# Kernel optimization log

Measured on AMD Instinct MI355X. Metric: run time of the kernel, lower is better.

The kernel has to match this reference:

```python
import math
import jax, jax.numpy as jnp
import numpy as np

C = 64
GRID = 2

def _conv1x1(x, W, b):
    # 1x1 conv == channel-mixing matmul: [B,C,H,W] x [O,C] -> [B,O,H,W]
    return jnp.einsum('bchw,oc->bohw', x, W) + b[None, :, None, None]

def setup_inputs() -> dict:
    key = jax.random.key(0)
    ks = jax.random.split(key, 11)
    s = 1.0 / math.sqrt(C)
    def w(k):
        return jax.random.normal(k, (C, C), dtype=jnp.float32) * s
    def bias(k):
        return jax.random.normal(k, (C,), dtype=jnp.float32) * 0.02
    return {
        'x': jax.random.normal(ks[0], (2, C, 128, 128), dtype=jnp.float32),
        'Wq': w(ks[1]), 'bq': bias(ks[2]),
        'Wk': w(ks[3]), 'bk': bias(ks[4]),
        'Wa': w(ks[5]), 'ba': bias(ks[6]),
        'Wb': w(ks[7]), 'bb': bias(ks[8]),
        'Wo': w(ks[9]), 'bo': bias(ks[10]),
    }

def reference(x, Wq, bq, Wk, bk, Wa, ba, Wb, bb, Wo, bo):
    B, c, H, W = x.shape
    g = GRID
    rh, rw = H // g, W // g  # H,W chosen divisible by grid -> no reflect pad
    N = rh * rw
    R = g * g

    q = _conv1x1(x, Wq, bq)
    k = _conv1x1(x, Wk, bk)
    a = _conv1x1(x, Wa, ba)
    bt = _conv1x1(x, Wb, bb)

    def regionize(t):
        # [B,C,H,W] -> [B, R, C, N] with N = rh*rw row-major per region
        return t.reshape(B, c, g, rh, g, rw).transpose(0, 2, 4, 1, 3, 5).reshape(B, R, c, N)

    qr, kr, ar, br = regionize(q), regionize(k), regionize(a), regionize(bt)

    # attn[b,r,n,m] = softmax_m( q^T k / sqrt(C) )
    attn = jax.nn.softmax(jnp.einsum('brcn,brcm->brnm', qr, kr) / math.sqrt(c), axis=-1)

    # out_r = alpha @ attn + beta @ attn^T
    out = (jnp.einsum('brcj,brjm->brcm', ar, attn)
           + jnp.einsum('brcj,brmj->brcm', br, attn))

    # [B,R,C,N] -> [B,C,H,W]
    out = out.reshape(B, g, g, c, rh, rw).transpose(0, 3, 1, 4, 2, 5).reshape(B, c, H, W)
    return _conv1x1(out, Wo, bo)
```

## Files before the change

### kernel.cpp

```cpp
#include <hip/hip_runtime.h>


typedef __attribute__((ext_vector_type(8)))  short bf16x8;
typedef __attribute__((ext_vector_type(16))) float f32x16;

#define MFMA32(a, b, c) __builtin_amdgcn_mfma_f32_32x32x16_bf16(a, b, c, 0, 0, 0)

constexpr int REG_ELEMS = 4096 * 64;
constexpr size_t QP_OFF    = 0;
constexpr size_t KP_OFF    = 4u  << 20;
constexpr size_t ATL_OFF   = 8u  << 20;
constexpr size_t BTL_OFF   = 12u << 20;
constexpr size_t OUTP_OFF  = 16u << 20;
constexpr size_t LNV_OFF   = 20u << 20;
constexpr size_t LPART_OFF = (20u << 20) + (128u << 10);

constexpr float QSCALE = 0.18033688011112042f;

__device__ __forceinline__ short f2bf(float f) {
    union { float f; unsigned u; } v; v.f = f;
    unsigned r = v.u + 0x7fffu + ((v.u >> 16) & 1u);
    return (short)(r >> 16);
}
__device__ __forceinline__ float bf2f(short s) {
    union { unsigned u; float f; } v; v.u = ((unsigned)(unsigned short)s) << 16;
    return v.f;
}
__device__ __forceinline__ unsigned fbits(float f) {
    union { float f; unsigned u; } v; v.f = f; return v.u;
}
__device__ __forceinline__ unsigned pack_trunc(float e0, float e1) {
    return __builtin_amdgcn_perm(fbits(e1), fbits(e0), 0x07060302u);
}
__device__ __forceinline__ f32x16 zero16() {
    f32x16 z;
    #pragma unroll
    for (int i = 0; i < 16; ++i) z[i] = 0.f;
    return z;
}
__device__ __forceinline__ float fexp2(float x) {
#if __has_builtin(__builtin_amdgcn_exp2f)
    return __builtin_amdgcn_exp2f(x);
#else
    return exp2f(x);
#endif
}
__device__ __forceinline__ void permswap32(unsigned& a, unsigned& b, bool hi) {
#if __has_builtin(__builtin_amdgcn_permlane32_swap)
    auto r = __builtin_amdgcn_permlane32_swap(a, b, false, false);
    a = r[0]; b = r[1];
#elif __has_builtin(__builtin_amdgcn_permlane32_swap_b32)
    auto r = __builtin_amdgcn_permlane32_swap_b32(a, b, false, false);
    a = r[0]; b = r[1];
#else
    unsigned ax = (unsigned)__shfl_xor((int)a, 32);
    unsigned bx = (unsigned)__shfl_xor((int)b, 32);
    unsigned na = hi ? bx : a;
    unsigned nb = hi ? b  : ax;
    a = na; b = nb;
#endif
}

typedef __attribute__((address_space(1))) const unsigned char as1_t;
typedef __attribute__((address_space(3))) unsigned char as3_t;
__device__ __forceinline__ void stage16(const void* g, void* l) {
    __builtin_amdgcn_global_load_lds((as1_t*)g, (as3_t*)l, 16, 0, 0);
}

__global__ __launch_bounds__(256) void k_conv_in(
    const float* __restrict__ x,
    const float* __restrict__ Wq, const float* __restrict__ bq,
    const float* __restrict__ Wk, const float* __restrict__ bk,
    const float* __restrict__ Wa, const float* __restrict__ ba,
    const float* __restrict__ Wb, const float* __restrict__ bb,
    char* __restrict__ ws)
{
    const int tid  = threadIdx.x;
    const int blk  = blockIdx.x;
    const int wseg = blk & 1;
    const int h    = (blk >> 1) & 127;
    const int b    = blk >> 8;
    const int br   = b * 4 + (h >> 6) * 2 + wseg;
    const int n0   = (h & 63) * 64;

    __shared__ float xs[64][68];
    __shared__ short trans[2][64][72];

    const float* xp = x + ((size_t)b * 64 * 16384) + (size_t)h * 128 + wseg * 64;
    #pragma unroll
    for (int r = 0; r < 4; ++r) {
        int idx = r * 256 + tid;
        int c   = idx >> 4;
        int w4  = (idx & 15) << 2;
        *(float4*)&xs[c][w4] = *(const float4*)(xp + (size_t)c * 16384 + w4);
    }
    __syncthreads();

    const int lane = tid & 63;
    const int wid  = tid >> 6;
    const int col  = lane & 31;
    const int l5   = lane >> 5;
    const int pH   = wid & 1;
    const int oH   = wid >> 1;
    const int px   = pH * 32 + col;
    const int oc   = oH * 32 + col;

    bf16x8 xhi[4], xlo[4];
    #pragma unroll
    for (int s = 0; s < 4; ++s) {
        union { bf16x8 v; short sh[8]; } uh, ul;
        #pragma unroll
        for (int e = 0; e < 8; ++e) {
            float xv = xs[s * 16 + l5 * 8 + e][px];
            short hh = f2bf(xv);
            uh.sh[e] = hh;
            ul.sh[e] = f2bf(xv - bf2f(hh));
        }
        xhi[s] = uh.v; xlo[s] = ul.v;
    }

    #pragma unroll
    for (int mat = 0; mat < 4; ++mat) {
        const float* Wsel = (mat == 0) ? Wq : (mat == 1) ? Wk : (mat == 2) ? Wa : Wb;
        const float* bsel = (mat == 0) ? bq : (mat == 1) ? bk : (mat == 2) ? ba : bb;

        bf16x8 whi[4], wlo[4];
        const float* wrow = Wsel + (size_t)oc * 64;
        #pragma unroll
        for (int s = 0; s < 4; ++s) {
            float4 f0 = *(const float4*)(wrow + s * 16 + l5 * 8);
            float4 f1 = *(const float4*)(wrow + s * 16 + l5 * 8 + 4);
            float wf[8] = { f0.x, f0.y, f0.z, f0.w, f1.x, f1.y, f1.z, f1.w };
            union { bf16x8 v; short sh[8]; } uh, ul;
            #pragma unroll
            for (int e = 0; e < 8; ++e) {
                short hh = f2bf(wf[e]);
                uh.sh[e] = hh;
                ul.sh[e] = f2bf(wf[e] - bf2f(hh));
            }
            whi[s] = uh.v; wlo[s] = ul.v;
        }

        f32x16 d = zero16();
        #pragma unroll
        for (int s = 0; s < 4; ++s) {
            d = MFMA32(xhi[s], whi[s], d);
            d = MFMA32(xhi[s], wlo[s], d);
            d = MFMA32(xlo[s], whi[s], d);
        }

        const float bias = bsel[oc];
        if (mat < 2) {
            const float sc = (mat == 0) ? QSCALE : 1.0f;
            #pragma unroll
            for (int r = 0; r < 16; ++r) {
                int pxl = pH * 32 + (r & 3) + 8 * (r >> 2) + 4 * l5;
                trans[mat][pxl][oc] = f2bf((d[r] + bias) * sc);
            }
        } else {
            short* base = (short*)(ws + (mat == 2 ? ATL_OFF : BTL_OFF))
                          + (size_t)br * REG_ELEMS;
            const int sw   = (oc >> 1) & 3;
            const int tile = (n0 >> 5) + pH;
            #pragma unroll
            for (int q = 0; q < 4; ++q) {
                short tmp4[4];
                #pragma unroll
                for (int rr = 0; rr < 4; ++rr) tmp4[rr] = f2bf(d[4 * q + rr] + bias);
                int segp = q ^ sw;
                short* p = base + (size_t)tile * 2048 + oc * 32 + segp * 8 + 4 * l5;
                *(uint2*)p = *(uint2*)tmp4;
            }
        }
    }
    __syncthreads();

    #pragma unroll
    for (int rep = 0; rep < 4; ++rep) {
        int idx  = rep * 256 + tid;
        int mat2 = idx >> 9;
        int row  = (idx >> 3) & 63;
        int seg  = idx & 7;
        short* dst = (short*)(ws + (mat2 ? KP_OFF : QP_OFF))
                     + (size_t)br * REG_ELEMS + (size_t)(n0 + row) * 64
                     + (seg ^ (row & 7)) * 8;
        *(uint4*)dst = *(uint4*)&trans[mat2][row][seg * 8];
    }
}

__global__ __launch_bounds__(256, 2) void k_stats(char* __restrict__ ws)
{
    const int tid  = threadIdx.x;
    const int br   = blockIdx.x & 7;
    const int nt   = (blockIdx.x >> 3) & 63;
    const int ms   = blockIdx.x >> 9;
    const int lane = tid & 63;
    const int w    = tid >> 6;
    const int wn   = w & 1;
    const int wi   = w >> 1;
    const int col  = lane & 31;
    const int l5   = lane >> 5;

    const short* Qb  = (const short*)(ws + QP_OFF) + (size_t)br * REG_ELEMS;
    const char*  Kbb = ws + KP_OFF + (size_t)br * REG_ELEMS * 2
                       + (size_t)ms * 262144;

    __shared__ __align__(16) char smem[16896];

    const int nrow = nt * 64 + wn * 32 + col;
    bf16x8 afr[4];
    #pragma unroll
    for (int s = 0; s < 4; ++s)
        afr[s] = *(const bf16x8*)(Qb + (size_t)nrow * 64 + (((2*s+l5) ^ (col & 7)) * 8));

    float sm[16];
    #pragma unroll
    for (int r = 0; r < 16; ++r) sm[r] = 0.f;

    {
        const char* g = Kbb + (size_t)w * 2048 + lane * 16;
        char* l = smem + w * 2048;
        stage16(g, l); stage16(g + 1024, l + 1024);
    }

    #pragma unroll 2
    for (int slab = 0; slab < 32; ++slab) {
        __syncthreads();
        if (slab + 1 < 32) {
            const char* g = Kbb + (size_t)(slab + 1) * 8192 + w * 2048 + lane * 16;
            char* l = smem + ((slab + 1) & 1) * 8192 + w * 2048;
            stage16(g, l); stage16(g + 1024, l + 1024);
        }
        const short* Ks = (const short*)(smem + (slab & 1) * 8192);
        f32x16 d = zero16();
        #pragma unroll
        for (int s = 0; s < 4; ++s) {
            bf16x8 bf = *(const bf16x8*)(Ks + (wi * 32 + col) * 64
                                         + ((2*s+l5) ^ (col & 7)) * 8);
            d = MFMA32(afr[s], bf, d);
        }
        #pragma unroll
        for (int r = 0; r < 16; ++r) sm[r] += fexp2(d[r]);
    }

    #pragma unroll
    for (int off = 1; off < 32; off <<= 1)
        #pragma unroll
        for (int r = 0; r < 16; ++r) sm[r] += __shfl_xor(sm[r], off);

    __syncthreads();
    float* Lred = (float*)(smem + 16384);
    if (col == 0) {
        #pragma unroll
        for (int r = 0; r < 16; ++r)
            Lred[w * 32 + ((r & 3) + 8 * (r >> 2) + 4 * l5)] = sm[r];
    }
    __syncthreads();
    if (tid < 64) {
        int wn2 = tid >> 5, nl = tid & 31;
        float L = Lred[wn2 * 32 + nl] + Lred[(wn2 + 2) * 32 + nl];
        ((float*)(ws + LPART_OFF))[(size_t)ms * 32768 + (size_t)br * 4096
                                   + nt * 64 + tid] = L;
    }
}

__global__ __launch_bounds__(256) void k_ascale(char* __restrict__ ws)
{
    const int tid = threadIdx.x;
    const int br  = blockIdx.x & 7;
    const int nt  = blockIdx.x >> 3;

    __shared__ float Larr[64];

    if (tid < 64) {
        const float* Lp = (const float*)(ws + LPART_OFF);
        const size_t idx = (size_t)br * 4096 + nt * 64 + tid;
        float li = 1.0f / (Lp[idx] + Lp[32768 + idx]);
        Larr[tid] = li;
        ((float*)(ws + LNV_OFF))[idx] = li;
    }
    __syncthreads();

    short* Ab = (short*)(ws + ATL_OFF) + (size_t)br * REG_ELEMS + (size_t)nt * 4096;
    #pragma unroll
    for (int rep = 0; rep < 2; ++rep) {
        int id = rep * 256 + tid;
        int t = id >> 8, c = (id >> 2) & 63, s = id & 3;
        int sg = s ^ ((c >> 1) & 3);
        int jl = t * 32 + sg * 8;
        short* p = Ab + (size_t)t * 2048 + c * 32 + s * 8;
        uint4 v = *(uint4*)p;
        short* sp = (short*)&v;
        short o[8];
        #pragma unroll
        for (int e = 0; e < 8; ++e) o[e] = f2bf(bf2f(sp[e]) * Larr[jl + e]);
        *(uint4*)p = *(uint4*)o;
    }
}

__global__ __launch_bounds__(256, 2) void k_attn(char* __restrict__ ws)
{
    const int tid  = threadIdx.x;
    const int br   = blockIdx.x & 7;
    const int mt   = blockIdx.x >> 3;
    const int lane = tid & 63;
    const int w    = tid >> 6;
    const int wj   = w & 1;
    const int jsw  = w >> 1;
    const int col  = lane & 31;
    const int l5   = lane >> 5;
    const bool hi  = (l5 != 0);

    const char* Qbb = ws + QP_OFF  + (size_t)br * REG_ELEMS * 2;
    const char* Kbb = ws + KP_OFF  + (size_t)br * REG_ELEMS * 2;
    const char* Abb = ws + ATL_OFF + (size_t)br * REG_ELEMS * 2;
    const char* Bbb = ws + BTL_OFF + (size_t)br * REG_ELEMS * 2;
    const float* Lnv = (const float*)(ws + LNV_OFF) + (size_t)br * 4096;
    short* OutPb    = (short*)(ws + OUTP_OFF) + (size_t)br * REG_ELEMS;

    __shared__ __align__(16) char smem[65536];

    const short* msrcb = (const short*)(wj == 0 ? Kbb : Qbb);
    bf16x8 mf[2][4];
    #pragma unroll
    for (int h = 0; h < 2; ++h) {
        const short* mr = msrcb + (size_t)(mt * 64 + h * 32 + col) * 64;
        #pragma unroll
        for (int s = 0; s < 4; ++s)
            mf[h][s] = *(const bf16x8*)(mr + ((2*s+l5) ^ (col & 7)) * 8);
    }

    f32x16 acc00 = zero16(), acc01 = zero16();
    f32x16 acc10 = zero16(), acc11 = zero16();

    const char* gsb = (w == 0) ? Qbb : (w == 1) ? Kbb : (w == 2) ? Abb : Bbb;

    {
        #pragma unroll
        for (int h = 0; h < 2; ++h) {
            const char* g = gsb + (size_t)h * 262144 + lane * 16;
            char* l = smem + h * 16384 + w * 4096 + lane * 16;
            #pragma unroll
            for (int i = 0; i < 4; ++i) stage16(g + i * 1024, l + i * 1024);
        }
    }

    #pragma unroll 2
    for (int rnd = 0; rnd < 64; ++rnd) {
        __syncthreads();
        if (rnd + 1 < 64) {
            #pragma unroll
            for (int h = 0; h < 2; ++h) {
                const char* g = gsb + (size_t)h * 262144
                                + (size_t)(rnd + 1) * 4096 + lane * 16;
                char* l = smem + ((rnd + 1) & 1) * 32768 + h * 16384
                          + w * 4096 + lane * 16;
                #pragma unroll
                for (int i = 0; i < 4; ++i) stage16(g + i * 1024, l + i * 1024);
            }
        }
        const char* sb = smem + (rnd & 1) * 32768 + jsw * 16384;
        const short* jr = (const short*)(sb + (wj == 0 ? 0 : 4096));
        const short* ts = (const short*)(sb + (wj == 0 ? 8192 : 12288));

        bf16x8 a[4];
        #pragma unroll
        for (int s = 0; s < 4; ++s)
            a[s] = *(const bf16x8*)(jr + col * 64 + ((2*s+l5) ^ (col & 7)) * 8);

        f32x16 d0 = zero16(), d1 = zero16();
        #pragma unroll
        for (int s = 0; s < 4; ++s) {
            d0 = MFMA32(a[s], mf[0][s], d0);
            d1 = MFMA32(a[s], mf[1][s], d1);
        }

        unsigned W0[8], W1[8];
        #pragma unroll
        for (int q = 0; q < 4; ++q) {
            W0[2*q]   = pack_trunc(fexp2(d0[4*q]),   fexp2(d0[4*q+1]));
            W0[2*q+1] = pack_trunc(fexp2(d0[4*q+2]), fexp2(d0[4*q+3]));
            W1[2*q]   = pack_trunc(fexp2(d1[4*q]),   fexp2(d1[4*q+1]));
            W1[2*q+1] = pack_trunc(fexp2(d1[4*q+2]), fexp2(d1[4*q+3]));
        }

        #pragma unroll
        for (int k16 = 0; k16 < 2; ++k16) {
            unsigned u0 = W0[4*k16+0], u1 = W0[4*k16+1];
            unsigned u2 = W0[4*k16+2], u3 = W0[4*k16+3];
            permswap32(u0, u2, hi);
            permswap32(u1, u3, hi);
            union { uint4 u; bf16x8 v; } fr0;
            fr0.u.x = u0; fr0.u.y = u1; fr0.u.z = u2; fr0.u.w = u3;

            unsigned v0 = W1[4*k16+0], v1 = W1[4*k16+1];
            unsigned v2 = W1[4*k16+2], v3 = W1[4*k16+3];
            permswap32(v0, v2, hi);
            permswap32(v1, v3, hi);
            union { uint4 u; bf16x8 v; } fr1;
            fr1.u.x = v0; fr1.u.y = v1; fr1.u.z = v2; fr1.u.w = v3;

            const int swz = ((2*k16 + l5) ^ ((col >> 1) & 3)) * 8;
            bf16x8 bL = *(const bf16x8*)(ts + col * 32 + swz);
            bf16x8 bH = *(const bf16x8*)(ts + (col + 32) * 32 + swz);
            acc00 = MFMA32(fr0.v, bL, acc00);
            acc01 = MFMA32(fr0.v, bH, acc01);
            acc10 = MFMA32(fr1.v, bL, acc10);
            acc11 = MFMA32(fr1.v, bH, acc11);
        }
    }

    __syncthreads();
    float* red = (float*)smem;
    if (w == 0) {
        #pragma unroll
        for (int h = 0; h < 2; ++h)
            #pragma unroll
            for (int r = 0; r < 16; ++r) {
                int ml = h * 32 + (r & 3) + 8 * (r >> 2) + 4 * l5;
                red[ml * 68 + col]      = h ? acc10[r] : acc00[r];
                red[ml * 68 + 32 + col] = h ? acc11[r] : acc01[r];
            }
    }
    __syncthreads();
    if (w == 2) {
        #pragma unroll
        for (int h = 0; h < 2; ++h)
            #pragma unroll
            for (int r = 0; r < 16; ++r) {
                int ml = h * 32 + (r & 3) + 8 * (r >> 2) + 4 * l5;
                red[ml * 68 + col]      += h ? acc10[r] : acc00[r];
                red[ml * 68 + 32 + col] += h ? acc11[r] : acc01[r];
            }
    }
    __syncthreads();
    if (w == 1) {
        #pragma unroll
        for (int h = 0; h < 2; ++h)
            #pragma unroll
            for (int r = 0; r < 16; ++r) {
                int ml = h * 32 + (r & 3) + 8 * (r >> 2) + 4 * l5;
                float li = Lnv[mt * 64 + ml];
                red[ml * 68 + col]      += li * (h ? acc10[r] : acc00[r]);
                red[ml * 68 + 32 + col] += li * (h ? acc11[r] : acc01[r]);
            }
    }
    __syncthreads();
    if (w == 3) {
        #pragma unroll
        for (int h = 0; h < 2; ++h)
            #pragma unroll
            for (int r = 0; r < 16; ++r) {
                int ml = h * 32 + (r & 3) + 8 * (r >> 2) + 4 * l5;
                float li = Lnv[mt * 64 + ml];
                red[ml * 68 + col]      += li * (h ? acc10[r] : acc00[r]);
                red[ml * 68 + 32 + col] += li * (h ? acc11[r] : acc01[r]);
            }
    }
    __syncthreads();
    {
        const int m  = tid >> 2;
        const int c0 = (tid & 3) * 16;
        const float* rp = red + m * 68 + c0;
        uint4 p0, p1;
        p0.x = pack_trunc(rp[0],  rp[1]);  p0.y = pack_trunc(rp[2],  rp[3]);
        p0.z = pack_trunc(rp[4],  rp[5]);  p0.w = pack_trunc(rp[6],  rp[7]);
        p1.x = pack_trunc(rp[8],  rp[9]);  p1.y = pack_trunc(rp[10], rp[11]);
        p1.z = pack_trunc(rp[12], rp[13]); p1.w = pack_trunc(rp[14], rp[15]);
        short* orow = OutPb + (size_t)(mt * 64 + m) * 64 + c0;
        *(uint4*)orow       = p0;
        *(uint4*)(orow + 8) = p1;
    }
}

__global__ __launch_bounds__(256) void k_conv_out(
    const char* __restrict__ ws,
    const float* __restrict__ Wo, const float* __restrict__ bo,
    float* __restrict__ out)
{
    const int tid  = threadIdx.x;
    const int lane = tid & 63;
    const int sub  = tid >> 6;
    const int blk  = blockIdx.x;
    const int br   = blk & 7;
    const int nt   = (blk >> 3) * 4 + sub;
    const int col  = lane & 31;
    const int l5   = lane >> 5;

    const short* OutPb = (const short*)(ws + OUTP_OFF) + (size_t)br * REG_ELEMS;

    bf16x8 afr[4];
    const short* arow = OutPb + (size_t)(nt * 32 + col) * 64 + l5 * 8;
    #pragma unroll
    for (int s = 0; s < 4; ++s) afr[s] = *(const bf16x8*)(arow + s * 16);

    bf16x8 bw[2][4];
    #pragma unroll
    for (int oh = 0; oh < 2; ++oh) {
        const float* wrow = Wo + (size_t)(oh * 32 + col) * 64 + l5 * 8;
        #pragma unroll
        for (int s = 0; s < 4; ++s) {
            float4 f0 = *(const float4*)(wrow + s * 16);
            float4 f1 = *(const float4*)(wrow + s * 16 + 4);
            union { bf16x8 v; short sh[8]; } u;
            u.sh[0] = f2bf(f0.x); u.sh[1] = f2bf(f0.y);
            u.sh[2] = f2bf(f0.z); u.sh[3] = f2bf(f0.w);
            u.sh[4] = f2bf(f1.x); u.sh[5] = f2bf(f1.y);
            u.sh[6] = f2bf(f1.z); u.sh[7] = f2bf(f1.w);
            bw[oh][s] = u.v;
        }
    }

    f32x16 d0 = zero16(), d1 = zero16();
    #pragma unroll
    for (int s = 0; s < 4; ++s) {
        d0 = MFMA32(afr[s], bw[0][s], d0);
        d1 = MFMA32(afr[s], bw[1][s], d1);
    }

    const int b  = br >> 2;
    const int gi = (br >> 1) & 1;
    const int gj = br & 1;

    #pragma unroll
    for (int oh = 0; oh < 2; ++oh) {
        const int oc = oh * 32 + col;
        const float bias = bo[oc];
        const f32x16& d = oh ? d1 : d0;
        #pragma unroll
        for (int q = 0; q < 4; ++q) {
            int nloc = 8 * q + 4 * l5;
            int nreg = nt * 32 + nloc;
            int wp   = nreg & 63;
            int ip   = nreg >> 6;
            float4 v = make_float4(d[4*q+0] + bias, d[4*q+1] + bias,
                                   d[4*q+2] + bias, d[4*q+3] + bias);
            float* op = out + ((size_t)(b * 64 + oc)) * 16384
                        + (size_t)(gi * 64 + ip) * 128 + gj * 64 + wp;
            *(float4*)op = v;
        }
    }
}

extern "C" void kernel_launch(void* const* d_in, const int* in_sizes, int n_in,
                              void* d_out, int out_size, void* d_ws, size_t ws_size,
                              hipStream_t stream)
{
    const float* x  = (const float*)d_in[0];
    const float* Wq = (const float*)d_in[1];
    const float* bq = (const float*)d_in[2];
    const float* Wk = (const float*)d_in[3];
    const float* bk = (const float*)d_in[4];
    const float* Wa = (const float*)d_in[5];
    const float* ba = (const float*)d_in[6];
    const float* Wb = (const float*)d_in[7];
    const float* bb = (const float*)d_in[8];
    const float* Wo = (const float*)d_in[9];
    const float* bo = (const float*)d_in[10];
    char* ws   = (char*)d_ws;
    float* out = (float*)d_out;

    hipLaunchKernelGGL(k_conv_in,  dim3(512),  dim3(256), 0, stream,
                       x, Wq, bq, Wk, bk, Wa, ba, Wb, bb, ws);
    hipLaunchKernelGGL(k_stats,    dim3(1024), dim3(256), 0, stream, ws);
    hipLaunchKernelGGL(k_ascale,   dim3(512),  dim3(256), 0, stream, ws);
    hipLaunchKernelGGL(k_attn,     dim3(512),  dim3(256), 0, stream, ws);
    hipLaunchKernelGGL(k_conv_out, dim3(256),  dim3(256), 0, stream,
                       ws, Wo, bo, out);
}
```

Measured before the change: 204.4 us.

## Double k_attn block to 512 threads covering 128 rows to share staged tiles

k_attn now runs 512-thread blocks over 256 blocks. Each block covers 128 output rows instead of 64, with the upper four waves taking the second 64-row half. Each staged Q/K/A/B round in LDS is shared by twice as many output rows, which halves the global-to-LDS traffic per output. The cost is a stricter register budget from launch_bounds(512,2), which could cause spills, and coarser grid granularity with fewer blocks.

```diff
diff --git a/kernel.cpp b/kernel.cpp
--- a/kernel.cpp
+++ b/kernel.cpp
@@ -298,7 +298,7 @@
     }
 }
 
-__global__ __launch_bounds__(256, 2) void k_attn(char* __restrict__ ws)
+__global__ __launch_bounds__(512, 2) void k_attn(char* __restrict__ ws)
 {
     const int tid  = threadIdx.x;
     const int br   = blockIdx.x & 7;
@@ -306,7 +306,8 @@
     const int lane = tid & 63;
     const int w    = tid >> 6;
     const int wj   = w & 1;
-    const int jsw  = w >> 1;
+    const int jsw  = (w >> 1) & 1;
+    const int mh   = w >> 2;
     const int col  = lane & 31;
     const int l5   = lane >> 5;
     const bool hi  = (l5 != 0);
@@ -324,7 +325,7 @@
     bf16x8 mf[2][4];
     #pragma unroll
     for (int h = 0; h < 2; ++h) {
-        const short* mr = msrcb + (size_t)(mt * 64 + h * 32 + col) * 64;
+        const short* mr = msrcb + (size_t)(mt * 128 + mh * 64 + h * 32 + col) * 64;
         #pragma unroll
         for (int s = 0; s < 4; ++s)
             mf[h][s] = *(const bf16x8*)(mr + ((2*s+l5) ^ (col & 7)) * 8);
@@ -333,31 +334,27 @@
     f32x16 acc00 = zero16(), acc01 = zero16();
     f32x16 acc10 = zero16(), acc11 = zero16();
 
-    const char* gsb = (w == 0) ? Qbb : (w == 1) ? Kbb : (w == 2) ? Abb : Bbb;
+    const int tt = w & 3;
+    const int hh = w >> 2;
+    const char* gsb = (tt == 0) ? Qbb : (tt == 1) ? Kbb : (tt == 2) ? Abb : Bbb;
 
     {
-        #pragma unroll
-        for (int h = 0; h < 2; ++h) {
-            const char* g = gsb + (size_t)h * 262144 + lane * 16;
-            char* l = smem + h * 16384 + w * 4096 + lane * 16;
-            #pragma unroll
-            for (int i = 0; i < 4; ++i) stage16(g + i * 1024, l + i * 1024);
-        }
+        const char* g = gsb + (size_t)hh * 262144 + lane * 16;
+        char* l = smem + hh * 16384 + tt * 4096 + lane * 16;
+        #pragma unroll
+        for (int i = 0; i < 4; ++i) stage16(g + i * 1024, l + i * 1024);
     }
 
     #pragma unroll 2
     for (int rnd = 0; rnd < 64; ++rnd) {
         __syncthreads();
         if (rnd + 1 < 64) {
-            #pragma unroll
-            for (int h = 0; h < 2; ++h) {
-                const char* g = gsb + (size_t)h * 262144
-                                + (size_t)(rnd + 1) * 4096 + lane * 16;
-                char* l = smem + ((rnd + 1) & 1) * 32768 + h * 16384
-                          + w * 4096 + lane * 16;
-                #pragma unroll
-                for (int i = 0; i < 4; ++i) stage16(g + i * 1024, l + i * 1024);
-            }
+            const char* g = gsb + (size_t)hh * 262144
+                            + (size_t)(rnd + 1) * 4096 + lane * 16;
+            char* l = smem + ((rnd + 1) & 1) * 32768 + hh * 16384
+                      + tt * 4096 + lane * 16;
+            #pragma unroll
+            for (int i = 0; i < 4; ++i) stage16(g + i * 1024, l + i * 1024);
         }
         const char* sb = smem + (rnd & 1) * 32768 + jsw * 16384;
         const short* jr = (const short*)(sb + (wj == 0 ? 0 : 4096));
@@ -412,47 +409,48 @@
 
     __syncthreads();
     float* red = (float*)smem;
-    if (w == 0) {
+    const int low2 = w & 3;
+    if (low2 == 0) {
         #pragma unroll
         for (int h = 0; h < 2; ++h)
             #pragma unroll
             for (int r = 0; r < 16; ++r) {
-                int ml = h * 32 + (r & 3) + 8 * (r >> 2) + 4 * l5;
+                int ml = mh * 64 + h * 32 + (r & 3) + 8 * (r >> 2) + 4 * l5;
                 red[ml * 68 + col]      = h ? acc10[r] : acc00[r];
                 red[ml * 68 + 32 + col] = h ? acc11[r] : acc01[r];
             }
     }
     __syncthreads();
-    if (w == 2) {
+    if (low2 == 2) {
         #pragma unroll
         for (int h = 0; h < 2; ++h)
             #pragma unroll
             for (int r = 0; r < 16; ++r) {
-                int ml = h * 32 + (r & 3) + 8 * (r >> 2) + 4 * l5;
+                int ml = mh * 64 + h * 32 + (r & 3) + 8 * (r >> 2) + 4 * l5;
                 red[ml * 68 + col]      += h ? acc10[r] : acc00[r];
                 red[ml * 68 + 32 + col] += h ? acc11[r] : acc01[r];
             }
     }
     __syncthreads();
-    if (w == 1) {
+    if (low2 == 1) {
         #pragma unroll
         for (int h = 0; h < 2; ++h)
             #pragma unroll
             for (int r = 0; r < 16; ++r) {
-                int ml = h * 32 + (r & 3) + 8 * (r >> 2) + 4 * l5;
-                float li = Lnv[mt * 64 + ml];
+                int ml = mh * 64 + h * 32 + (r & 3) + 8 * (r >> 2) + 4 * l5;
+                float li = Lnv[mt * 128 + ml];
                 red[ml * 68 + col]      += li * (h ? acc10[r] : acc00[r]);
                 red[ml * 68 + 32 + col] += li * (h ? acc11[r] : acc01[r]);
             }
     }
     __syncthreads();
-    if (w == 3) {
+    if (low2 == 3) {
         #pragma unroll
         for (int h = 0; h < 2; ++h)
             #pragma unroll
             for (int r = 0; r < 16; ++r) {
-                int ml = h * 32 + (r & 3) + 8 * (r >> 2) + 4 * l5;
-                float li = Lnv[mt * 64 + ml];
+                int ml = mh * 64 + h * 32 + (r & 3) + 8 * (r >> 2) + 4 * l5;
+                float li = Lnv[mt * 128 + ml];
                 red[ml * 68 + col]      += li * (h ? acc10[r] : acc00[r]);
                 red[ml * 68 + 32 + col] += li * (h ? acc11[r] : acc01[r]);
             }
@@ -467,7 +465,7 @@
         p0.z = pack_trunc(rp[4],  rp[5]);  p0.w = pack_trunc(rp[6],  rp[7]);
         p1.x = pack_trunc(rp[8],  rp[9]);  p1.y = pack_trunc(rp[10], rp[11]);
         p1.z = pack_trunc(rp[12], rp[13]); p1.w = pack_trunc(rp[14], rp[15]);
-        short* orow = OutPb + (size_t)(mt * 64 + m) * 64 + c0;
+        short* orow = OutPb + (size_t)(mt * 128 + m) * 64 + c0;
         *(uint4*)orow       = p0;
         *(uint4*)(orow + 8) = p1;
     }
@@ -564,7 +562,7 @@
                        x, Wq, bq, Wk, bk, Wa, ba, Wb, bb, ws);
     hipLaunchKernelGGL(k_stats,    dim3(1024), dim3(256), 0, stream, ws);
     hipLaunchKernelGGL(k_ascale,   dim3(512),  dim3(256), 0, stream, ws);
-    hipLaunchKernelGGL(k_attn,     dim3(512),  dim3(256), 0, stream, ws);
+    hipLaunchKernelGGL(k_attn,     dim3(256),  dim3(512), 0, stream, ws);
     hipLaunchKernelGGL(k_conv_out, dim3(256),  dim3(256), 0, stream,
                        ws, Wo, bo, out);
 }
```

After: 197.9 us. -3.2%, faster.
